# Kernel tuning notes

Measured on AMD Instinct MI355X. Metric: run time of the kernel, lower is better.

Reference implementation:

```python
import jax, jax.numpy as jnp
import numpy as np

N_NODES = 100000
N_EDGES = 1600000
F_IN = 256
HID = 128
N_CLS = 64
K_APPNP = 10
ALPHA = 0.1


def setup_inputs() -> dict:
    key = jax.random.key(0)
    ks = jax.random.split(key, 12)
    x = jax.random.normal(ks[0], (N_NODES, F_IN), dtype=jnp.float32)
    edge_index = jax.random.randint(ks[1], (2, N_EDGES), 0, N_NODES, dtype=jnp.int64)
    def lin(k, fan_in, fan_out):
        s = 1.0 / np.sqrt(fan_in)
        kw, kb = jax.random.split(k)
        W = jax.random.uniform(kw, (fan_in, fan_out), minval=-s, maxval=s, dtype=jnp.float32)
        b = jax.random.uniform(kb, (fan_out,), minval=-s, maxval=s, dtype=jnp.float32)
        return W, b
    W1, b1 = lin(ks[2], F_IN, HID)
    W2, b2 = lin(ks[3], HID, HID)
    Wc, bc = lin(ks[4], HID, N_CLS)
    We, be = lin(ks[5], N_CLS, N_CLS)
    return {"x": x, "edge_index": edge_index, "W1": W1, "b1": b1, "W2": W2,
            "b2": b2, "Wc": Wc, "bc": bc, "We": We, "be": be}


def reference(x, edge_index, W1, b1, W2, b2, Wc, bc, We, be):
    N = x.shape[0]
    loop = jnp.arange(N)
    row = jnp.concatenate([edge_index[0], loop])  # source nodes (+ self loops)
    col = jnp.concatenate([edge_index[1], loop])  # target nodes (+ self loops)
    # symmetric GCN normalization: deg computed on targets
    deg = jax.ops.segment_sum(jnp.ones_like(col, dtype=x.dtype), col, num_segments=N)
    dinv = jnp.where(deg > 0, jax.lax.rsqrt(deg), 0.0)
    norm = dinv[row] * dinv[col]  # [E+N]

    def prop(h):  # normalized scatter-add aggregation
        return jax.ops.segment_sum(h[row] * norm[:, None], col, num_segments=N)

    # GCNConv: transform -> propagate -> bias (dropout is eval no-op)
    h = jax.nn.relu(prop(x @ W1) + b1)
    h = jax.nn.relu(prop(h @ W2) + b2)
    logits = h @ Wc + bc
    ev = jax.nn.relu(logits @ We + be)
    # APPNP: z_{k+1} = (1-alpha) * A_hat z_k + alpha * ev
    z = ev
    for _ in range(K_APPNP):
        z = (1.0 - ALPHA) * prop(z) + ALPHA * ev
    return jax.nn.log_softmax(z, axis=1)
```

## Files before the change

### kernel.cpp

```cpp
#include <hip/hip_runtime.h>
#include <hip/hip_fp16.h>


struct __align__(16) half8 { __half2 h[4]; };
typedef _Float16 f16x8 __attribute__((ext_vector_type(8)));
typedef float f32x4 __attribute__((ext_vector_type(4)));

__device__ __forceinline__ f16x8 cvt8(const float4& a, const float4& b) {
    f16x8 r;
    r[0] = (_Float16)a.x; r[1] = (_Float16)a.y; r[2] = (_Float16)a.z; r[3] = (_Float16)a.w;
    r[4] = (_Float16)b.x; r[5] = (_Float16)b.y; r[6] = (_Float16)b.z; r[7] = (_Float16)b.w;
    return r;
}

__global__ __launch_bounds__(256) void k_init(int* deg, int N) {
    int i = blockIdx.x * 256 + threadIdx.x;
    if (i < N) deg[i] = 1;
}

__global__ __launch_bounds__(256) void k_count(const int* __restrict__ dst,
                                               int* deg, int* __restrict__ rank, int E) {
    int e = blockIdx.x * 256 + threadIdx.x;
    if (e < E) {
        int r = atomicAdd(&deg[dst[e]], 1);
        rank[e] = r - 1;
    }
}

__global__ __launch_bounds__(256) void k_scanA(const int* __restrict__ deg, int* bs, int N) {
    __shared__ int s[256];
    int t = threadIdx.x;
    int i = blockIdx.x * 256 + t;
    int c = (i < N) ? (deg[i] - 1) : 0;
    s[t] = c; __syncthreads();
    for (int o = 128; o > 0; o >>= 1) {
        if (t < o) s[t] += s[t + o];
        __syncthreads();
    }
    if (t == 0) bs[blockIdx.x] = s[0];
}

__global__ __launch_bounds__(512) void k_scanB(int* bs, int NB) {
    __shared__ int s[512];
    int t = threadIdx.x;
    int v = (t < NB) ? bs[t] : 0;
    s[t] = v; __syncthreads();
    for (int o = 1; o < 512; o <<= 1) {
        int u = (t >= o) ? s[t - o] : 0;
        __syncthreads();
        s[t] += u;
        __syncthreads();
    }
    if (t < NB) bs[t] = s[t] - v;
}

__global__ __launch_bounds__(256) void k_scanC(const int* __restrict__ deg, const int* __restrict__ bs,
                                               int* row_ptr, float* dinv, int N) {
    __shared__ int s[256];
    int t = threadIdx.x;
    int i = blockIdx.x * 256 + t;
    int c = (i < N) ? (deg[i] - 1) : 0;
    s[t] = c; __syncthreads();
    for (int o = 1; o < 256; o <<= 1) {
        int u = (t >= o) ? s[t - o] : 0;
        __syncthreads();
        s[t] += u;
        __syncthreads();
    }
    if (i < N) {
        int off = bs[blockIdx.x];
        row_ptr[i] = off + s[t] - c;
        dinv[i] = rsqrtf((float)deg[i]);
        if (i == N - 1) row_ptr[N] = off + s[t];
    }
}

__global__ __launch_bounds__(256) void k_fill(const int* __restrict__ src, const int* __restrict__ dst,
                                              const int* __restrict__ row_ptr,
                                              const int* __restrict__ rank,
                                              int* __restrict__ csr_src, int E) {
    int e = blockIdx.x * 256 + threadIdx.x;
    if (e < E) csr_src[row_ptr[dst[e]] + rank[e]] = src[e];
}

__global__ __launch_bounds__(256) void k_fuseW(const float* __restrict__ Wc,
                                               const float* __restrict__ bc,
                                               const float* __restrict__ We,
                                               const float* __restrict__ be,
                                               float* __restrict__ Wf,
                                               float* __restrict__ bf) {
    __shared__ float sWe[64 * 64];
    int tid = threadIdx.x;
    for (int i = tid; i < 64 * 64 / 4; i += 256)
        ((float4*)sWe)[i] = ((const float4*)We)[i];
    __syncthreads();
    for (int idx = tid; idx < 128 * 64; idx += 256) {
        int r = idx >> 6, c = idx & 63;
        float s = 0.f;
#pragma unroll 8
        for (int j = 0; j < 64; j++) s += Wc[r * 64 + j] * sWe[j * 64 + c];
        Wf[idx] = s;
    }
    if (tid < 64) {
        float s = be[tid];
#pragma unroll 8
        for (int j = 0; j < 64; j++) s += bc[j] * sWe[j * 64 + tid];
        bf[tid] = s;
    }
}

__global__ __launch_bounds__(256) void k_prepW2(const float* __restrict__ W,
                                                __half* __restrict__ Wt, int K, int NCOL) {
    int idx = blockIdx.x * 256 + threadIdx.x;
    if (idx >= K * NCOL) return;
    int j = idx & 7;
    int n = (idx >> 3) % NCOL;
    int qk = idx / (8 * NCOL);
    int quad = qk & 3, kc = qk >> 2;
    int k = kc * 32 + quad * 8 + j;
    Wt[idx] = __float2half(W[k * NCOL + n]);
}

template <int K, bool IN_F16>
__global__ __launch_bounds__(512, 4) void k_gemm(const void* __restrict__ Xv,
                                                 const __half* __restrict__ Wtf,
                                                 const float* __restrict__ dinv,
                                                 __half* __restrict__ Y, int N) {
    constexpr int NK = K / 32;
    constexpr int ITER = K / 32;
    __shared__ __align__(16) __half sB[K * 128];

    const int tid = threadIdx.x;
    const int wv = tid >> 6, ln = tid & 63;
    const int m = ln & 15, quad = ln >> 4;
    const int rowBase = blockIdx.x * 128 + wv * 16;
    int rowA = rowBase + m;
    if (rowA > N - 1) rowA = N - 1;

    const float*  xf = (const float*)Xv;
    const __half* xh = (const __half*)Xv;
    const long aOff = (long)rowA * K + quad * 8;

    f16x8 a8[4];
    float4 t0[4], t1[4];
    if constexpr (IN_F16) {
#pragma unroll
        for (int kc = 0; kc < NK; ++kc)
            a8[kc] = *(const f16x8*)&xh[aOff + kc * 32];
    } else {
#pragma unroll
        for (int c = 0; c < 4; ++c) {
            t0[c] = *(const float4*)&xf[aOff + c * 32];
            t1[c] = *(const float4*)&xf[aOff + c * 32 + 4];
        }
    }

    {
        f16x8 tb[ITER];
        const f16x8* g = (const f16x8*)Wtf;
#pragma unroll
        for (int i = 0; i < ITER; ++i) tb[i] = g[(i * 8 + wv) * 64 + ln];
        f16x8* l = (f16x8*)sB;
#pragma unroll
        for (int i = 0; i < ITER; ++i) l[(i * 8 + wv) * 64 + ln] = tb[i];
    }
    __syncthreads();

    if constexpr (!IN_F16) {
#pragma unroll
        for (int c = 0; c < 4; ++c) a8[c] = cvt8(t0[c], t1[c]);
#pragma unroll
        for (int c = 0; c < 4; ++c) {
            t0[c] = *(const float4*)&xf[aOff + (c + 4) * 32];
            t1[c] = *(const float4*)&xf[aOff + (c + 4) * 32 + 4];
        }
    }

    f32x4 d[8];
#pragma unroll
    for (int ct = 0; ct < 8; ++ct) d[ct] = {0.f, 0.f, 0.f, 0.f};

#pragma unroll
    for (int h = 0; h < NK / 4; ++h) {
        if constexpr (!IN_F16) {
            if (h == 1) {
#pragma unroll
                for (int c = 0; c < 4; ++c) a8[c] = cvt8(t0[c], t1[c]);
            }
        }
#pragma unroll
        for (int kq = 0; kq < 4; ++kq) {
            const int kc = h * 4 + kq;
            const f16x8 a = a8[IN_F16 ? kc : kq];
            const __half* bb = &sB[(size_t)(kc * 4 + quad) * 128 * 8];
#pragma unroll
            for (int ct = 0; ct < 8; ++ct) {
                const f16x8 b = *(const f16x8*)&bb[(ct * 16 + m) * 8];
                d[ct] = __builtin_amdgcn_mfma_f32_16x16x32_f16(a, b, d[ct], 0, 0, 0);
            }
        }
    }

#pragma unroll
    for (int ct = 0; ct < 8; ++ct) {
        const int col = ct * 16 + m;
#pragma unroll
        for (int reg = 0; reg < 4; ++reg) {
            const int row = rowBase + quad * 4 + reg;
            if (row < N)
                Y[(long)row * 128 + col] = __float2half(d[ct][reg] * dinv[row]);
        }
    }
}

__global__ __launch_bounds__(512, 4) void k_cls(const __half* __restrict__ H,
                                                const __half* __restrict__ Wtf,
                                                const float* __restrict__ bf,
                                                const float* __restrict__ dinv,
                                                float* __restrict__ ev,
                                                __half* __restrict__ evs, int N) {
    __shared__ __align__(16) __half sB[128 * 64];
    const int tid = threadIdx.x;
    const int wv = tid >> 6, ln = tid & 63;
    const int m = ln & 15, quad = ln >> 4;
    const int rowBase = blockIdx.x * 128 + wv * 16;
    int rowA = rowBase + m;
    if (rowA > N - 1) rowA = N - 1;
    const long aOff = (long)rowA * 128 + quad * 8;

    f16x8 a8[4];
#pragma unroll
    for (int kc = 0; kc < 4; ++kc)
        a8[kc] = *(const f16x8*)&H[aOff + kc * 32];

    {
        f16x8 tb[2];
        const f16x8* g = (const f16x8*)Wtf;
#pragma unroll
        for (int i = 0; i < 2; ++i) tb[i] = g[(i * 8 + wv) * 64 + ln];
        f16x8* l = (f16x8*)sB;
#pragma unroll
        for (int i = 0; i < 2; ++i) l[(i * 8 + wv) * 64 + ln] = tb[i];
    }
    __syncthreads();

    f32x4 d[4];
#pragma unroll
    for (int ct = 0; ct < 4; ++ct) d[ct] = {0.f, 0.f, 0.f, 0.f};

#pragma unroll
    for (int kc = 0; kc < 4; ++kc) {
        const __half* bb = &sB[(size_t)(kc * 4 + quad) * 64 * 8];
#pragma unroll
        for (int ct = 0; ct < 4; ++ct) {
            const f16x8 b = *(const f16x8*)&bb[(ct * 16 + m) * 8];
            d[ct] = __builtin_amdgcn_mfma_f32_16x16x32_f16(a8[kc], b, d[ct], 0, 0, 0);
        }
    }

#pragma unroll
    for (int ct = 0; ct < 4; ++ct) {
        const int col = ct * 16 + m;
#pragma unroll
        for (int reg = 0; reg < 4; ++reg) {
            const int row = rowBase + quad * 4 + reg;
            if (row < N) {
                float v = fmaxf(d[ct][reg] + bf[col], 0.f);
                ev[(long)row * 64 + col] = v;
                evs[(long)row * 64 + col] = __float2half(v * dinv[row]);
            }
        }
    }
}

template <int F, int MODE>
__global__ __launch_bounds__(256) void k_prop2(const __half* __restrict__ tab,
                                               const int* __restrict__ row_ptr,
                                               const int* __restrict__ csr_src,
                                               const float* __restrict__ dinv,
                                               const float* __restrict__ bias,
                                               const void* __restrict__ evx,
                                               void* __restrict__ out, int N) {
    constexpr int LPE = F / 8;
    constexpr int S = 64 / LPE;
    int wave = threadIdx.x >> 6;
    int lane = threadIdx.x & 63;
    int node = blockIdx.x * 4 + wave;
    if (node >= N) return;
    int slot = lane / LPE;
    int fl = lane % LPE;
    const int2 se = *(const int2*)&row_ptr[node];
    int s = se.x, e = se.y;

    float acc[8], accB[8];
#pragma unroll
    for (int q = 0; q < 8; q++) { acc[q] = 0.f; accB[q] = 0.f; }

    int j = s + slot;
    int i0 = 0, i1 = 0;
    if (j < e) i0 = csr_src[j];
    if (j + S < e) i1 = csr_src[j + S];
    while (j + S < e) {
        const int jn = j + 2 * S;
        int n0 = 0, n1 = 0;
        if (jn < e) n0 = csr_src[jn];
        if (jn + S < e) n1 = csr_src[jn + S];
        const half8 a = *(const half8*)&tab[(long)i0 * F + 8 * fl];
        const half8 b = *(const half8*)&tab[(long)i1 * F + 8 * fl];
#pragma unroll
        for (int q = 0; q < 4; q++) {
            float2 fa = __half22float2(a.h[q]);
            float2 fb = __half22float2(b.h[q]);
            acc[2 * q] += fa.x; acc[2 * q + 1] += fa.y;
            accB[2 * q] += fb.x; accB[2 * q + 1] += fb.y;
        }
        i0 = n0; i1 = n1; j = jn;
    }
    if (j < e) {
        const half8 a = *(const half8*)&tab[(long)i0 * F + 8 * fl];
#pragma unroll
        for (int q = 0; q < 4; q++) {
            float2 fa = __half22float2(a.h[q]);
            acc[2 * q] += fa.x; acc[2 * q + 1] += fa.y;
        }
    }
    if (slot == 0) {
        const half8 a = *(const half8*)&tab[(long)node * F + 8 * fl];
#pragma unroll
        for (int q = 0; q < 4; q++) {
            float2 fa = __half22float2(a.h[q]);
            acc[2 * q] += fa.x; acc[2 * q + 1] += fa.y;
        }
    }
#pragma unroll
    for (int q = 0; q < 8; q++) acc[q] += accB[q];

#pragma unroll
    for (int off = LPE; off < 64; off <<= 1) {
#pragma unroll
        for (int q = 0; q < 8; q++) acc[q] += __shfl_xor(acc[q], off, 64);
    }

    if (slot == 0) {
        float di = dinv[node];
        if (MODE == 3) {
            const float4 b0 = *(const float4*)&bias[8 * fl];
            const float4 b1 = *(const float4*)&bias[8 * fl + 4];
            half8 ov;
            ov.h[0] = __floats2half2_rn(fmaxf(di * acc[0] + b0.x, 0.f),
                                        fmaxf(di * acc[1] + b0.y, 0.f));
            ov.h[1] = __floats2half2_rn(fmaxf(di * acc[2] + b0.z, 0.f),
                                        fmaxf(di * acc[3] + b0.w, 0.f));
            ov.h[2] = __floats2half2_rn(fmaxf(di * acc[4] + b1.x, 0.f),
                                        fmaxf(di * acc[5] + b1.y, 0.f));
            ov.h[3] = __floats2half2_rn(fmaxf(di * acc[6] + b1.z, 0.f),
                                        fmaxf(di * acc[7] + b1.w, 0.f));
            *(half8*)&((__half*)out)[(long)node * F + 8 * fl] = ov;
        } else if (MODE == 1) {
            float d2 = 0.9f * di * di;
            const half8 eh = *(const half8*)&((const __half*)evx)[(long)node * F + 8 * fl];
            half8 ov;
#pragma unroll
            for (int q = 0; q < 4; q++) {
                float2 ef = __half22float2(eh.h[q]);
                float vx = d2 * acc[2 * q] + 0.1f * ef.x;
                float vy = d2 * acc[2 * q + 1] + 0.1f * ef.y;
                ov.h[q] = __floats2half2_rn(vx, vy);
            }
            *(half8*)&((__half*)out)[(long)node * F + 8 * fl] = ov;
        } else {
            float d1 = 0.9f * di;
            const float* ef = (const float*)evx + (long)node * F + 8 * fl;
            const float4 e0 = *(const float4*)ef;
            const float4 e1 = *(const float4*)(ef + 4);
            float v[8];
            v[0] = d1 * acc[0] + 0.1f * e0.x;
            v[1] = d1 * acc[1] + 0.1f * e0.y;
            v[2] = d1 * acc[2] + 0.1f * e0.z;
            v[3] = d1 * acc[3] + 0.1f * e0.w;
            v[4] = d1 * acc[4] + 0.1f * e1.x;
            v[5] = d1 * acc[5] + 0.1f * e1.y;
            v[6] = d1 * acc[6] + 0.1f * e1.z;
            v[7] = d1 * acc[7] + 0.1f * e1.w;
            float m = v[0];
#pragma unroll
            for (int q = 1; q < 8; q++) m = fmaxf(m, v[q]);
#pragma unroll
            for (int off = 1; off < LPE; off <<= 1) m = fmaxf(m, __shfl_xor(m, off, 64));
            float ssum = 0.f;
#pragma unroll
            for (int q = 0; q < 8; q++) ssum += __expf(v[q] - m);
#pragma unroll
            for (int off = 1; off < LPE; off <<= 1) ssum += __shfl_xor(ssum, off, 64);
            float lse = m + __logf(ssum);
            float* o = (float*)out + (long)node * F + 8 * fl;
            float4 v0, v1;
            v0.x = v[0] - lse; v0.y = v[1] - lse; v0.z = v[2] - lse; v0.w = v[3] - lse;
            v1.x = v[4] - lse; v1.y = v[5] - lse; v1.z = v[6] - lse; v1.w = v[7] - lse;
            *(float4*)o = v0;
            *(float4*)(o + 4) = v1;
        }
    }
}

extern "C" void kernel_launch(void* const* d_in, const int* in_sizes, int n_in,
                              void* d_out, int out_size, void* d_ws, size_t ws_size,
                              hipStream_t stream) {
    const float* x  = (const float*)d_in[0];
    const int* edges = (const int*)d_in[1];
    const float* W1 = (const float*)d_in[2];
    const float* b1 = (const float*)d_in[3];
    const float* W2 = (const float*)d_in[4];
    const float* b2 = (const float*)d_in[5];
    const float* Wc = (const float*)d_in[6];
    const float* bc = (const float*)d_in[7];
    const float* We = (const float*)d_in[8];
    const float* be = (const float*)d_in[9];

    const int N = in_sizes[0] / 256;
    const int E = in_sizes[1] / 2;
    const int* esrc = edges;
    const int* edst = edges + E;

    char* ws = (char*)d_ws;
    size_t off = 0;
    auto alloc = [&](size_t bytes) -> void* {
        void* p = ws + off;
        off += (bytes + 255) & ~(size_t)255;
        return p;
    };
    int*    deg     = (int*)alloc((size_t)N * 4);
    int*    row_ptr = (int*)alloc((size_t)(N + 1) * 4);
    float*  dinv    = (float*)alloc((size_t)N * 4);
    int*    bs      = (int*)alloc(4096 * 4);
    int*    rank    = (int*)alloc((size_t)E * 4);
    int*    csr_src = (int*)alloc((size_t)E * 4);
    __half* P       = (__half*)alloc((size_t)N * 128 * 2);
    __half* Q16     = (__half*)alloc((size_t)N * 128 * 2);
    __half* zA      = (__half*)alloc((size_t)N * 64 * 2);
    __half* zB      = (__half*)alloc((size_t)N * 64 * 2);
    __half* evs     = (__half*)alloc((size_t)N * 64 * 2);
    float*  Wf      = (float*)alloc(128 * 64 * 4);
    float*  bf      = (float*)alloc(64 * 4);
    __half* W1t     = (__half*)alloc(128 * 256 * 2);
    __half* W2t     = (__half*)alloc(128 * 128 * 2);
    __half* Wft     = (__half*)alloc(64 * 128 * 2);
    float*  ev      = (float*)d_out;

    const int nbN = (N + 255) / 256;
    const int nbE = (E + 255) / 256;
    const int nbP = (N + 3) / 4;
    const int TG  = (N + 127) / 128;

    k_init<<<nbN, 256, 0, stream>>>(deg, N);
    k_count<<<nbE, 256, 0, stream>>>(edst, deg, rank, E);
    k_fuseW<<<1, 256, 0, stream>>>(Wc, bc, We, be, Wf, bf);
    k_prepW2<<<(256 * 128 + 255) / 256, 256, 0, stream>>>(W1, W1t, 256, 128);
    k_prepW2<<<(128 * 128 + 255) / 256, 256, 0, stream>>>(W2, W2t, 128, 128);
    k_prepW2<<<(128 * 64 + 255) / 256, 256, 0, stream>>>(Wf, Wft, 128, 64);
    k_scanA<<<nbN, 256, 0, stream>>>(deg, bs, N);
    k_scanB<<<1, 512, 0, stream>>>(bs, nbN);
    k_scanC<<<nbN, 256, 0, stream>>>(deg, bs, row_ptr, dinv, N);
    k_fill<<<nbE, 256, 0, stream>>>(esrc, edst, row_ptr, rank, csr_src, E);

    k_gemm<256, false><<<TG, 512, 0, stream>>>(x, W1t, dinv, P, N);
    k_prop2<128, 3><<<nbP, 256, 0, stream>>>(P, row_ptr, csr_src, dinv, b1, nullptr, Q16, N);

    k_gemm<128, true><<<TG, 512, 0, stream>>>(Q16, W2t, dinv, P, N);
    k_prop2<128, 3><<<nbP, 256, 0, stream>>>(P, row_ptr, csr_src, dinv, b2, nullptr, Q16, N);

    k_cls<<<TG, 512, 0, stream>>>(Q16, Wft, bf, dinv, ev, evs, N);

    const __half* zin = evs;
    __half* zout;
    for (int it = 0; it < 9; ++it) {
        zout = (it % 2 == 0) ? zA : zB;
        k_prop2<64, 1><<<nbP, 256, 0, stream>>>(zin, row_ptr, csr_src, dinv, nullptr, evs, zout, N);
        zin = zout;
    }
    k_prop2<64, 2><<<nbP, 256, 0, stream>>>(zin, row_ptr, csr_src, dinv, nullptr, ev, (float*)d_out, N);
}
```

Measured before the change: 972.3 us.

## Overlap edge degree counting with first GEMM and merge weight prep kernels

The degree-counting atomics now run as extra blocks of the first GEMM launch. That GEMM therefore no longer needs dinv, so it writes unscaled outputs, and a new prop mode applies the source dinv per gathered neighbor instead. The weight conversion and fusion kernels are merged into one launch, and the init kernel becomes a memset, cutting launch count and letting the atomic scatter overlap MFMA work. The cost is an extra dinv gather per edge in the first propagation, plus mixing heterogeneous blocks within one launch.

```diff
diff --git a/kernel.cpp b/kernel.cpp
--- a/kernel.cpp
+++ b/kernel.cpp
@@ -13,25 +13,11 @@
     return r;
 }
 
-__global__ __launch_bounds__(256) void k_init(int* deg, int N) {
-    int i = blockIdx.x * 256 + threadIdx.x;
-    if (i < N) deg[i] = 1;
-}
-
-__global__ __launch_bounds__(256) void k_count(const int* __restrict__ dst,
-                                               int* deg, int* __restrict__ rank, int E) {
-    int e = blockIdx.x * 256 + threadIdx.x;
-    if (e < E) {
-        int r = atomicAdd(&deg[dst[e]], 1);
-        rank[e] = r - 1;
-    }
-}
-
 __global__ __launch_bounds__(256) void k_scanA(const int* __restrict__ deg, int* bs, int N) {
     __shared__ int s[256];
     int t = threadIdx.x;
     int i = blockIdx.x * 256 + t;
-    int c = (i < N) ? (deg[i] - 1) : 0;
+    int c = (i < N) ? deg[i] : 0;
     s[t] = c; __syncthreads();
     for (int o = 128; o > 0; o >>= 1) {
         if (t < o) s[t] += s[t + o];
@@ -59,7 +45,7 @@
     __shared__ int s[256];
     int t = threadIdx.x;
     int i = blockIdx.x * 256 + t;
-    int c = (i < N) ? (deg[i] - 1) : 0;
+    int c = (i < N) ? deg[i] : 0;
     s[t] = c; __syncthreads();
     for (int o = 1; o < 256; o <<= 1) {
         int u = (t >= o) ? s[t - o] : 0;
@@ -70,7 +56,7 @@
     if (i < N) {
         int off = bs[blockIdx.x];
         row_ptr[i] = off + s[t] - c;
-        dinv[i] = rsqrtf((float)deg[i]);
+        dinv[i] = rsqrtf((float)(deg[i] + 1));
         if (i == N - 1) row_ptr[N] = off + s[t];
     }
 }
@@ -83,49 +69,70 @@
     if (e < E) csr_src[row_ptr[dst[e]] + rank[e]] = src[e];
 }
 
-__global__ __launch_bounds__(256) void k_fuseW(const float* __restrict__ Wc,
-                                               const float* __restrict__ bc,
-                                               const float* __restrict__ We,
-                                               const float* __restrict__ be,
-                                               float* __restrict__ Wf,
-                                               float* __restrict__ bf) {
+__global__ __launch_bounds__(256) void k_prep(const float* __restrict__ W1,
+                                              const float* __restrict__ W2,
+                                              const float* __restrict__ Wc,
+                                              const float* __restrict__ bc,
+                                              const float* __restrict__ We,
+                                              const float* __restrict__ be,
+                                              __half* __restrict__ W1t,
+                                              __half* __restrict__ W2t,
+                                              __half* __restrict__ Wft,
+                                              float* __restrict__ bf) {
     __shared__ float sWe[64 * 64];
-    int tid = threadIdx.x;
-    for (int i = tid; i < 64 * 64 / 4; i += 256)
-        ((float4*)sWe)[i] = ((const float4*)We)[i];
-    __syncthreads();
-    for (int idx = tid; idx < 128 * 64; idx += 256) {
-        int r = idx >> 6, c = idx & 63;
-        float s = 0.f;
+    const int b = blockIdx.x, tid = threadIdx.x;
+    if (b < 128) {
+        int idx = b * 256 + tid;
+        int j = idx & 7, n = (idx >> 3) & 127, qk = idx >> 10;
+        int quad = qk & 3, kc = qk >> 2;
+        int k = kc * 32 + quad * 8 + j;
+        W1t[idx] = __float2half(W1[k * 128 + n]);
+    } else if (b < 192) {
+        int idx = (b - 128) * 256 + tid;
+        int j = idx & 7, n = (idx >> 3) & 127, qk = idx >> 10;
+        int quad = qk & 3, kc = qk >> 2;
+        int k = kc * 32 + quad * 8 + j;
+        W2t[idx] = __float2half(W2[k * 128 + n]);
+    } else {
+        for (int i = tid; i < 64 * 64 / 4; i += 256)
+            ((float4*)sWe)[i] = ((const float4*)We)[i];
+        __syncthreads();
+        for (int idx = tid; idx < 128 * 64; idx += 256) {
+            int r = idx >> 6, c = idx & 63;
+            float s = 0.f;
 #pragma unroll 8
-        for (int j = 0; j < 64; j++) s += Wc[r * 64 + j] * sWe[j * 64 + c];
-        Wf[idx] = s;
-    }
-    if (tid < 64) {
-        float s = be[tid];
+            for (int j = 0; j < 64; j++) s += Wc[r * 64 + j] * sWe[j * 64 + c];
+            int kc = r >> 5, quad = (r >> 3) & 3, jj = r & 7;
+            Wft[(((kc * 4 + quad) * 64) + c) * 8 + jj] = __float2half(s);
+        }
+        if (tid < 64) {
+            float s = be[tid];
 #pragma unroll 8
-        for (int j = 0; j < 64; j++) s += bc[j] * sWe[j * 64 + tid];
-        bf[tid] = s;
-    }
-}
-
-__global__ __launch_bounds__(256) void k_prepW2(const float* __restrict__ W,
-                                                __half* __restrict__ Wt, int K, int NCOL) {
-    int idx = blockIdx.x * 256 + threadIdx.x;
-    if (idx >= K * NCOL) return;
-    int j = idx & 7;
-    int n = (idx >> 3) % NCOL;
-    int qk = idx / (8 * NCOL);
-    int quad = qk & 3, kc = qk >> 2;
-    int k = kc * 32 + quad * 8 + j;
-    Wt[idx] = __float2half(W[k * NCOL + n]);
-}
-
-template <int K, bool IN_F16>
+            for (int j = 0; j < 64; j++) s += bc[j] * sWe[j * 64 + tid];
+            bf[tid] = s;
+        }
+    }
+}
+
+template <int K, bool IN_F16, bool COUNT>
 __global__ __launch_bounds__(512, 4) void k_gemm(const void* __restrict__ Xv,
                                                  const __half* __restrict__ Wtf,
                                                  const float* __restrict__ dinv,
-                                                 __half* __restrict__ Y, int N) {
+                                                 __half* __restrict__ Y, int N,
+                                                 const int* __restrict__ dst,
+                                                 int* __restrict__ deg,
+                                                 int* __restrict__ rank,
+                                                 int E, int TG) {
+    if constexpr (COUNT) {
+        if (blockIdx.x >= TG) {
+            int e = (blockIdx.x - TG) * 512 + threadIdx.x;
+            if (e < E) {
+                int r = atomicAdd(&deg[dst[e]], 1);
+                rank[e] = r;
+            }
+            return;
+        }
+    }
     constexpr int NK = K / 32;
     constexpr int ITER = K / 32;
     __shared__ __align__(16) __half sB[K * 128];
@@ -207,8 +214,12 @@
 #pragma unroll
         for (int reg = 0; reg < 4; ++reg) {
             const int row = rowBase + quad * 4 + reg;
-            if (row < N)
-                Y[(long)row * 128 + col] = __float2half(d[ct][reg] * dinv[row]);
+            if (row < N) {
+                if constexpr (COUNT)
+                    Y[(long)row * 128 + col] = __float2half(d[ct][reg]);
+                else
+                    Y[(long)row * 128 + col] = __float2half(d[ct][reg] * dinv[row]);
+            }
         }
     }
 }
@@ -307,29 +318,50 @@
         if (jn + S < e) n1 = csr_src[jn + S];
         const half8 a = *(const half8*)&tab[(long)i0 * F + 8 * fl];
         const half8 b = *(const half8*)&tab[(long)i1 * F + 8 * fl];
+        if (MODE == 4) {
+            float da = dinv[i0], db = dinv[i1];
+#pragma unroll
+            for (int q = 0; q < 4; q++) {
+                float2 fa = __half22float2(a.h[q]);
+                float2 fb = __half22float2(b.h[q]);
+                acc[2 * q] += da * fa.x; acc[2 * q + 1] += da * fa.y;
+                accB[2 * q] += db * fb.x; accB[2 * q + 1] += db * fb.y;
+            }
+        } else {
+#pragma unroll
+            for (int q = 0; q < 4; q++) {
+                float2 fa = __half22float2(a.h[q]);
+                float2 fb = __half22float2(b.h[q]);
+                acc[2 * q] += fa.x; acc[2 * q + 1] += fa.y;
+                accB[2 * q] += fb.x; accB[2 * q + 1] += fb.y;
+            }
+        }
+        i0 = n0; i1 = n1; j = jn;
+    }
+    if (j < e) {
+        const half8 a = *(const half8*)&tab[(long)i0 * F + 8 * fl];
+        if (MODE == 4) {
+            float da = dinv[i0];
+#pragma unroll
+            for (int q = 0; q < 4; q++) {
+                float2 fa = __half22float2(a.h[q]);
+                acc[2 * q] += da * fa.x; acc[2 * q + 1] += da * fa.y;
+            }
+        } else {
+#pragma unroll
+            for (int q = 0; q < 4; q++) {
+                float2 fa = __half22float2(a.h[q]);
+                acc[2 * q] += fa.x; acc[2 * q + 1] += fa.y;
+            }
+        }
+    }
+    if (slot == 0) {
+        const half8 a = *(const half8*)&tab[(long)node * F + 8 * fl];
+        float ds = (MODE == 4) ? dinv[node] : 1.f;
 #pragma unroll
         for (int q = 0; q < 4; q++) {
             float2 fa = __half22float2(a.h[q]);
-            float2 fb = __half22float2(b.h[q]);
-            acc[2 * q] += fa.x; acc[2 * q + 1] += fa.y;
-            accB[2 * q] += fb.x; accB[2 * q + 1] += fb.y;
-        }
-        i0 = n0; i1 = n1; j = jn;
-    }
-    if (j < e) {
-        const half8 a = *(const half8*)&tab[(long)i0 * F + 8 * fl];
-#pragma unroll
-        for (int q = 0; q < 4; q++) {
-            float2 fa = __half22float2(a.h[q]);
-            acc[2 * q] += fa.x; acc[2 * q + 1] += fa.y;
-        }
-    }
-    if (slot == 0) {
-        const half8 a = *(const half8*)&tab[(long)node * F + 8 * fl];
-#pragma unroll
-        for (int q = 0; q < 4; q++) {
-            float2 fa = __half22float2(a.h[q]);
-            acc[2 * q] += fa.x; acc[2 * q + 1] += fa.y;
+            acc[2 * q] += ds * fa.x; acc[2 * q + 1] += ds * fa.y;
         }
     }
 #pragma unroll
@@ -343,7 +375,7 @@
 
     if (slot == 0) {
         float di = dinv[node];
-        if (MODE == 3) {
+        if (MODE == 3 || MODE == 4) {
             const float4 b0 = *(const float4*)&bias[8 * fl];
             const float4 b1 = *(const float4*)&bias[8 * fl + 4];
             half8 ov;
@@ -440,7 +472,6 @@
     __half* zA      = (__half*)alloc((size_t)N * 64 * 2);
     __half* zB      = (__half*)alloc((size_t)N * 64 * 2);
     __half* evs     = (__half*)alloc((size_t)N * 64 * 2);
-    float*  Wf      = (float*)alloc(128 * 64 * 4);
     float*  bf      = (float*)alloc(64 * 4);
     __half* W1t     = (__half*)alloc(128 * 256 * 2);
     __half* W2t     = (__half*)alloc(128 * 128 * 2);
@@ -451,22 +482,22 @@
     const int nbE = (E + 255) / 256;
     const int nbP = (N + 3) / 4;
     const int TG  = (N + 127) / 128;
-
-    k_init<<<nbN, 256, 0, stream>>>(deg, N);
-    k_count<<<nbE, 256, 0, stream>>>(edst, deg, rank, E);
-    k_fuseW<<<1, 256, 0, stream>>>(Wc, bc, We, be, Wf, bf);
-    k_prepW2<<<(256 * 128 + 255) / 256, 256, 0, stream>>>(W1, W1t, 256, 128);
-    k_prepW2<<<(128 * 128 + 255) / 256, 256, 0, stream>>>(W2, W2t, 128, 128);
-    k_prepW2<<<(128 * 64 + 255) / 256, 256, 0, stream>>>(Wf, Wft, 128, 64);
+    const int CB  = (E + 511) / 512;
+
+    hipMemsetAsync(deg, 0, (size_t)N * 4, stream);
+    k_prep<<<193, 256, 0, stream>>>(W1, W2, Wc, bc, We, be, W1t, W2t, Wft, bf);
+    k_gemm<256, false, true><<<TG + CB, 512, 0, stream>>>(x, W1t, nullptr, P, N,
+                                                          edst, deg, rank, E, TG);
+
     k_scanA<<<nbN, 256, 0, stream>>>(deg, bs, N);
     k_scanB<<<1, 512, 0, stream>>>(bs, nbN);
     k_scanC<<<nbN, 256, 0, stream>>>(deg, bs, row_ptr, dinv, N);
     k_fill<<<nbE, 256, 0, stream>>>(esrc, edst, row_ptr, rank, csr_src, E);
 
-    k_gemm<256, false><<<TG, 512, 0, stream>>>(x, W1t, dinv, P, N);
-    k_prop2<128, 3><<<nbP, 256, 0, stream>>>(P, row_ptr, csr_src, dinv, b1, nullptr, Q16, N);
-
-    k_gemm<128, true><<<TG, 512, 0, stream>>>(Q16, W2t, dinv, P, N);
+    k_prop2<128, 4><<<nbP, 256, 0, stream>>>(P, row_ptr, csr_src, dinv, b1, nullptr, Q16, N);
+
+    k_gemm<128, true, false><<<TG, 512, 0, stream>>>(Q16, W2t, dinv, P, N,
+                                                     nullptr, nullptr, nullptr, 0, TG);
     k_prop2<128, 3><<<nbP, 256, 0, stream>>>(P, row_ptr, csr_src, dinv, b2, nullptr, Q16, N);
 
     k_cls<<<TG, 512, 0, stream>>>(Q16, Wft, bf, dinv, ev, evs, N);
```

Result: faster. 941.3 us (-3.2%).
